# Performance work log

Hardware: AMD Instinct MI355X
Metric: run time of the kernel (lower is better)

## Reference

```python
import jax, jax.numpy as jnp
import numpy as np

N_NODES = 50000
N_EDGES = 800000
D = 256


def gcn_conv(x, edge_index, W, b, n_nodes):
    """PyG-style GCNConv: add self-loops, symmetric norm, linear, scatter-add."""
    # add self loops
    loops = jnp.arange(n_nodes, dtype=edge_index.dtype)
    src = jnp.concatenate([edge_index[0], loops])  # message sources
    dst = jnp.concatenate([edge_index[1], loops])  # aggregation targets
    # symmetric normalization: deg computed on targets (incl. self loops)
    deg = jax.ops.segment_sum(jnp.ones_like(dst, dtype=x.dtype), dst,
                              num_segments=n_nodes)
    dinv = jnp.where(deg > 0, jax.lax.rsqrt(deg), 0.0)
    norm = dinv[src] * dinv[dst]  # [E+N]
    h = x @ W  # [N, out]
    msg = h[src] * norm[:, None]  # gather + scale, [E+N, out]
    out = jax.ops.segment_sum(msg, dst, num_segments=n_nodes)  # scatter-add
    return out + b


def setup_inputs() -> dict:
    key = jax.random.key(0)
    k1, k2, k3, k4 = jax.random.split(key, 4)
    x = jax.random.normal(k1, (N_NODES, D), dtype=jnp.float32)
    edge_index = jax.random.randint(k2, (2, N_EDGES), 0, N_NODES, dtype=jnp.int64)
    s = 1.0 / np.sqrt(D)
    W1 = jax.random.normal(k3, (D, D), dtype=jnp.float32) * s
    W2 = jax.random.normal(k4, (D, D), dtype=jnp.float32) * s
    b1 = jnp.zeros((D,), dtype=jnp.float32)
    b2 = jnp.zeros((D,), dtype=jnp.float32)
    return {"x": x, "edge_index": edge_index, "W1": W1, "b1": b1,
            "W2": W2, "b2": b2}


def reference(x, edge_index, W1, b1, W2, b2):
    n = x.shape[0]
    out = gcn_conv(x, edge_index, W1, b1, n)
    out = jax.nn.relu(out)  # dropout is identity in eval mode (p=0.2 in train)
    out = out + gcn_conv(x, edge_index, W2, b2, n)
    return out
```

## Files before the change

### kernel.cpp

```cpp
#include <hip/hip_runtime.h>
#include <hip/hip_bf16.h>

#define DIM 256
#define CAP 64

typedef short bf16x8 __attribute__((ext_vector_type(8)));
typedef float f32x4  __attribute__((ext_vector_type(4)));

__device__ __forceinline__ unsigned short f2b(float f) {
    union { __hip_bfloat16 h; unsigned short u; } cv;
    cv.h = __float2bfloat16(f);
    return cv.u;
}
__device__ __forceinline__ float b2f(unsigned short u) {
    return __uint_as_float(((unsigned)u) << 16);
}

#define OFF_FILL   0
#define OFF_DINV   262144
#define OFF_WT1    524288
#define OFF_WT2    655360
#define OFF_BUCKET 786432
#define OFF_AGG    13631488
#define OFF_YB     39845888
#define NEED_BF    (OFF_YB + 25600000ull)

__global__ void k_fill(const int* __restrict__ src, const int* __restrict__ dst,
                       int* __restrict__ fill, int* __restrict__ bucket, int nE) {
    int e = blockIdx.x * blockDim.x + threadIdx.x;
    if (e < nE) {
        int d = dst[e];
        int pos = atomicAdd(&fill[d], 1);
        if (pos < CAP) bucket[d * CAP + pos] = src[e];
    }
}

__global__ void k_dinv(const int* __restrict__ fill, float* __restrict__ dinv, int n) {
    int i = blockIdx.x * blockDim.x + threadIdx.x;
    if (i < n) dinv[i] = rsqrtf((float)(1 + fill[i]));
}

__global__ void k_wt(const float* __restrict__ W1, const float* __restrict__ W2,
                     unsigned short* __restrict__ wt1, unsigned short* __restrict__ wt2) {
    int t = blockIdx.x * blockDim.x + threadIdx.x;
    if (t < DIM * DIM) {
        int k = t & 255, nn = t >> 8;
        wt1[t] = f2b(W1[k * DIM + nn]);
        wt2[t] = f2b(W2[k * DIM + nn]);
    }
}

__global__ void k_yb(const float4* __restrict__ x4, const float* __restrict__ dinv,
                     ushort4* __restrict__ yb, int n4) {
    int t = blockIdx.x * blockDim.x + threadIdx.x;
    if (t < n4) {
        float d = dinv[t >> 6];
        float4 v = x4[t];
        ushort4 r;
        r.x = f2b(d * v.x); r.y = f2b(d * v.y);
        r.z = f2b(d * v.z); r.w = f2b(d * v.w);
        yb[t] = r;
    }
}

__global__ void k_agg_bf(const ushort4* __restrict__ yb, const float* __restrict__ dinv,
                         const int* __restrict__ fill, const int* __restrict__ bucket,
                         ushort4* __restrict__ aggbf, int n) {
    int node = (blockIdx.x * blockDim.x + threadIdx.x) >> 6;
    int lane = threadIdx.x & 63;
    if (node >= n) return;

    ushort4 s = yb[(size_t)node * 64 + lane];
    float a0 = b2f(s.x), a1 = b2f(s.y), a2 = b2f(s.z), a3 = b2f(s.w);

    int c = fill[node];
    if (c > CAP) c = CAP;
    const int* bk = bucket + node * CAP;

    int k = 0;
    for (; k + 4 <= c; k += 4) {
        int4 j4 = *(const int4*)(bk + k);
        ushort4 r0 = yb[(size_t)j4.x * 64 + lane];
        ushort4 r1 = yb[(size_t)j4.y * 64 + lane];
        ushort4 r2 = yb[(size_t)j4.z * 64 + lane];
        ushort4 r3 = yb[(size_t)j4.w * 64 + lane];
        a0 += b2f(r0.x) + b2f(r1.x) + b2f(r2.x) + b2f(r3.x);
        a1 += b2f(r0.y) + b2f(r1.y) + b2f(r2.y) + b2f(r3.y);
        a2 += b2f(r0.z) + b2f(r1.z) + b2f(r2.z) + b2f(r3.z);
        a3 += b2f(r0.w) + b2f(r1.w) + b2f(r2.w) + b2f(r3.w);
    }
    for (; k < c; k++) {
        int j = bk[k];
        ushort4 r = yb[(size_t)j * 64 + lane];
        a0 += b2f(r.x); a1 += b2f(r.y); a2 += b2f(r.z); a3 += b2f(r.w);
    }

    float di = dinv[node];
    ushort4 r;
    r.x = f2b(a0 * di); r.y = f2b(a1 * di);
    r.z = f2b(a2 * di); r.w = f2b(a3 * di);
    unsigned long long rbits;
    __builtin_memcpy(&rbits, &r, 8);
    __builtin_nontemporal_store(rbits,
        (unsigned long long*)&aggbf[(size_t)node * 64 + lane]);
}

__global__ void k_agg_f32(const float4* __restrict__ x4, const float* __restrict__ dinv,
                          const int* __restrict__ fill, const int* __restrict__ bucket,
                          ushort4* __restrict__ aggbf, int n) {
    int node = (blockIdx.x * blockDim.x + threadIdx.x) >> 6;
    int lane = threadIdx.x & 63;
    if (node >= n) return;

    float di = dinv[node];
    float4 xi = x4[(size_t)node * 64 + lane];
    float a0 = di * xi.x, a1 = di * xi.y, a2 = di * xi.z, a3 = di * xi.w;

    int c = fill[node];
    if (c > CAP) c = CAP;
    const int* bk = bucket + node * CAP;
    for (int k = 0; k < c; k++) {
        int j = bk[k];
        float dj = dinv[j];
        float4 xj = x4[(size_t)j * 64 + lane];
        a0 += dj * xj.x; a1 += dj * xj.y; a2 += dj * xj.z; a3 += dj * xj.w;
    }
    ushort4 r;
    r.x = f2b(a0 * di); r.y = f2b(a1 * di);
    r.z = f2b(a2 * di); r.w = f2b(a3 * di);
    aggbf[(size_t)node * 64 + lane] = r;
}

__launch_bounds__(256, 2)
__global__ void k_gemm(const short* __restrict__ aggbf,
                       const short* __restrict__ wt1, const short* __restrict__ wt2,
                       const float* __restrict__ b1, const float* __restrict__ b2,
                       float* __restrict__ out, int n) {
    int mblk = blockIdx.x >> 1;
    int cb   = blockIdx.x & 1;
    int r0   = mblk * 64;
    int c0   = cb * 128;

    int wave = threadIdx.x >> 6;
    int lane = threadIdx.x & 63;
    int rowoff = (wave >> 1) * 32;
    int coloff = (wave & 1) * 64;
    int lrow = lane & 15;
    int quad = lane >> 4;

    int ar0 = r0 + rowoff + lrow;        if (ar0 >= n) ar0 = 0;
    int ar1 = r0 + rowoff + 16 + lrow;   if (ar1 >= n) ar1 = 0;
    const short* ap0 = aggbf + (size_t)ar0 * DIM + quad * 8;
    const short* ap1 = aggbf + (size_t)ar1 * DIM + quad * 8;

    const short* bp1[4];
    const short* bp2[4];
#pragma unroll
    for (int ct = 0; ct < 4; ct++) {
        int c = c0 + coloff + ct * 16 + lrow;
        bp1[ct] = wt1 + (size_t)c * DIM + quad * 8;
        bp2[ct] = wt2 + (size_t)c * DIM + quad * 8;
    }

    f32x4 acc1[2][4], acc2[2][4];
#pragma unroll
    for (int rt = 0; rt < 2; rt++)
#pragma unroll
        for (int ct = 0; ct < 4; ct++) {
            acc1[rt][ct] = (f32x4){0.f, 0.f, 0.f, 0.f};
            acc2[rt][ct] = (f32x4){0.f, 0.f, 0.f, 0.f};
        }

#pragma unroll
    for (int kk = 0; kk < DIM; kk += 32) {
        bf16x8 a0 = *(const bf16x8*)(ap0 + kk);
        bf16x8 a1 = *(const bf16x8*)(ap1 + kk);
#pragma unroll
        for (int ct = 0; ct < 4; ct++) {
            bf16x8 w1f = *(const bf16x8*)(bp1[ct] + kk);
            bf16x8 w2f = *(const bf16x8*)(bp2[ct] + kk);
            acc1[0][ct] = __builtin_amdgcn_mfma_f32_16x16x32_bf16(a0, w1f, acc1[0][ct], 0, 0, 0);
            acc1[1][ct] = __builtin_amdgcn_mfma_f32_16x16x32_bf16(a1, w1f, acc1[1][ct], 0, 0, 0);
            acc2[0][ct] = __builtin_amdgcn_mfma_f32_16x16x32_bf16(a0, w2f, acc2[0][ct], 0, 0, 0);
            acc2[1][ct] = __builtin_amdgcn_mfma_f32_16x16x32_bf16(a1, w2f, acc2[1][ct], 0, 0, 0);
        }
    }

#pragma unroll
    for (int ct = 0; ct < 4; ct++) {
        int col = c0 + coloff + ct * 16 + lrow;
        float bb1 = b1[col], bb2 = b2[col];
#pragma unroll
        for (int rt = 0; rt < 2; rt++) {
            int rbase = r0 + rowoff + rt * 16 + quad * 4;
#pragma unroll
            for (int i = 0; i < 4; i++) {
                int row = rbase + i;
                if (row < n) {
                    float v = fmaxf(acc1[rt][ct][i] + bb1, 0.f) + acc2[rt][ct][i] + bb2;
                    __builtin_nontemporal_store(v, &out[(size_t)row * DIM + col]);
                }
            }
        }
    }
}

extern "C" void kernel_launch(void* const* d_in, const int* in_sizes, int n_in,
                              void* d_out, int out_size, void* d_ws, size_t ws_size,
                              hipStream_t stream) {
    const float* x  = (const float*)d_in[0];
    const int*   ei = (const int*)d_in[1];
    const float* W1 = (const float*)d_in[2];
    const float* b1 = (const float*)d_in[3];
    const float* W2 = (const float*)d_in[4];
    const float* b2 = (const float*)d_in[5];
    float* out = (float*)d_out;

    int n = in_sizes[0] / DIM;
    int E = in_sizes[1] / 2;
    const int* src = ei;
    const int* dst = ei + E;

    char* ws = (char*)d_ws;
    int*            fill   = (int*)(ws + OFF_FILL);
    float*          dinv   = (float*)(ws + OFF_DINV);
    unsigned short* wt1    = (unsigned short*)(ws + OFF_WT1);
    unsigned short* wt2    = (unsigned short*)(ws + OFF_WT2);
    int*            bucket = (int*)(ws + OFF_BUCKET);
    ushort4*        aggbf  = (ushort4*)(ws + OFF_AGG);
    ushort4*        yb     = (ushort4*)(ws + OFF_YB);

    (void)hipMemsetAsync(fill, 0, n * sizeof(int), stream);

    k_fill<<<(E + 255) / 256, 256, 0, stream>>>(src, dst, fill, bucket, E);
    k_dinv<<<(n + 255) / 256, 256, 0, stream>>>(fill, dinv, n);
    k_wt  <<<(DIM * DIM + 255) / 256, 256, 0, stream>>>(W1, W2, wt1, wt2);

    int aggBlocks = (n * 64 + 255) / 256;
    bool use_bf = (ws_size >= NEED_BF);
    if (use_bf) {
        int n4 = n * DIM / 4;
        k_yb<<<(n4 + 255) / 256, 256, 0, stream>>>((const float4*)x, dinv, yb, n4);
        k_agg_bf<<<aggBlocks, 256, 0, stream>>>(yb, dinv, fill, bucket, aggbf, n);
    } else {
        k_agg_f32<<<aggBlocks, 256, 0, stream>>>((const float4*)x, dinv, fill, bucket, aggbf, n);
    }

    int mblocks = (n + 63) / 64;
    k_gemm<<<mblocks * 2, 256, 0, stream>>>((const short*)aggbf, (const short*)wt1,
                                            (const short*)wt2, b1, b2, out, n);
}
```

Baseline: 296.5 us.

## Stage weight slices in swizzled LDS and make GEMM persistent over row tiles

The GEMM kernel now loads a 64-column slice of both transposed weight matrices into LDS once per block, using an XOR swizzle to avoid bank conflicts. Each block then loops persistently over 128-row tiles with a grid of 128x4 blocks, and the A fragments for the next k-step are prefetched. This is meant to remove the repeated global/L2 weight fetches the old per-tile kernel issued, at the cost of 64KB of LDS per block and a fixed grid that may underfill the GPU or leave tiles unbalanced. The launch bounds also change to 4 blocks per CU.

```diff
diff --git a/kernel.cpp b/kernel.cpp
--- a/kernel.cpp
+++ b/kernel.cpp
@@ -3,6 +3,7 @@
 
 #define DIM 256
 #define CAP 64
+#define GEMM_G 128
 
 typedef short bf16x8 __attribute__((ext_vector_type(8)));
 typedef float f32x4  __attribute__((ext_vector_type(4)));
@@ -131,74 +132,94 @@
     aggbf[(size_t)node * 64 + lane] = r;
 }
 
-__launch_bounds__(256, 2)
+__launch_bounds__(256, 4)
 __global__ void k_gemm(const short* __restrict__ aggbf,
                        const short* __restrict__ wt1, const short* __restrict__ wt2,
                        const float* __restrict__ b1, const float* __restrict__ b2,
-                       float* __restrict__ out, int n) {
-    int mblk = blockIdx.x >> 1;
-    int cb   = blockIdx.x & 1;
-    int r0   = mblk * 64;
-    int c0   = cb * 128;
-
-    int wave = threadIdx.x >> 6;
-    int lane = threadIdx.x & 63;
-    int rowoff = (wave >> 1) * 32;
-    int coloff = (wave & 1) * 64;
+                       float* __restrict__ out, int n, int ntiles) {
+    __shared__ uint4 bs[4096];
+
+    int c0  = blockIdx.y * 64;
+    int tid = threadIdx.x;
+
+#pragma unroll
+    for (int i = 0; i < 16; i++) {
+        int l = tid + i * 256;
+        int m = l >> 11, rem = l & 2047, nn = rem >> 5, p = rem & 31;
+        const short* base = (m == 0) ? wt1 : wt2;
+        const uint4* sp = (const uint4*)(base + ((size_t)(c0 + nn)) * DIM) + p;
+        bs[(m << 11) + (nn << 5) + (p ^ (nn & 31))] = *sp;
+    }
+    __syncthreads();
+
+    int lane = tid & 63;
+    int wave = tid >> 6;
     int lrow = lane & 15;
     int quad = lane >> 4;
 
-    int ar0 = r0 + rowoff + lrow;        if (ar0 >= n) ar0 = 0;
-    int ar1 = r0 + rowoff + 16 + lrow;   if (ar1 >= n) ar1 = 0;
-    const short* ap0 = aggbf + (size_t)ar0 * DIM + quad * 8;
-    const short* ap1 = aggbf + (size_t)ar1 * DIM + quad * 8;
-
-    const short* bp1[4];
-    const short* bp2[4];
+    float bb1[4], bb2[4];
 #pragma unroll
     for (int ct = 0; ct < 4; ct++) {
-        int c = c0 + coloff + ct * 16 + lrow;
-        bp1[ct] = wt1 + (size_t)c * DIM + quad * 8;
-        bp2[ct] = wt2 + (size_t)c * DIM + quad * 8;
-    }
-
-    f32x4 acc1[2][4], acc2[2][4];
-#pragma unroll
-    for (int rt = 0; rt < 2; rt++)
-#pragma unroll
-        for (int ct = 0; ct < 4; ct++) {
-            acc1[rt][ct] = (f32x4){0.f, 0.f, 0.f, 0.f};
-            acc2[rt][ct] = (f32x4){0.f, 0.f, 0.f, 0.f};
+        bb1[ct] = b1[c0 + ct * 16 + lrow];
+        bb2[ct] = b2[c0 + ct * 16 + lrow];
+    }
+
+    for (int t = blockIdx.x; t < ntiles; t += gridDim.x) {
+        int rowbase = t * 128 + wave * 32;
+        int r0 = rowbase + lrow;       if (r0 >= n) r0 = 0;
+        int r1 = rowbase + 16 + lrow;  if (r1 >= n) r1 = 0;
+        const short* ap0 = aggbf + (size_t)r0 * DIM + quad * 8;
+        const short* ap1 = aggbf + (size_t)r1 * DIM + quad * 8;
+
+        f32x4 acc1[2][4], acc2[2][4];
+#pragma unroll
+        for (int sub = 0; sub < 2; sub++)
+#pragma unroll
+            for (int ct = 0; ct < 4; ct++) {
+                acc1[sub][ct] = (f32x4){0.f, 0.f, 0.f, 0.f};
+                acc2[sub][ct] = (f32x4){0.f, 0.f, 0.f, 0.f};
+            }
+
+        bf16x8 a0 = *(const bf16x8*)(ap0);
+        bf16x8 a1 = *(const bf16x8*)(ap1);
+#pragma unroll
+        for (int s = 0; s < 8; s++) {
+            bf16x8 na0 = a0, na1 = a1;
+            if (s < 7) {
+                na0 = *(const bf16x8*)(ap0 + (s + 1) * 32);
+                na1 = *(const bf16x8*)(ap1 + (s + 1) * 32);
+            }
+#pragma unroll
+            for (int ct = 0; ct < 4; ct++) {
+                int nn = ct * 16 + lrow;
+                int ch = (4 * s + quad) ^ (nn & 31);
+                uint4 u1 = bs[(nn << 5) + ch];
+                uint4 u2 = bs[2048 + (nn << 5) + ch];
+                bf16x8 w1f, w2f;
+                __builtin_memcpy(&w1f, &u1, 16);
+                __builtin_memcpy(&w2f, &u2, 16);
+                acc1[0][ct] = __builtin_amdgcn_mfma_f32_16x16x32_bf16(a0, w1f, acc1[0][ct], 0, 0, 0);
+                acc1[1][ct] = __builtin_amdgcn_mfma_f32_16x16x32_bf16(a1, w1f, acc1[1][ct], 0, 0, 0);
+                acc2[0][ct] = __builtin_amdgcn_mfma_f32_16x16x32_bf16(a0, w2f, acc2[0][ct], 0, 0, 0);
+                acc2[1][ct] = __builtin_amdgcn_mfma_f32_16x16x32_bf16(a1, w2f, acc2[1][ct], 0, 0, 0);
+            }
+            a0 = na0; a1 = na1;
         }
 
 #pragma unroll
-    for (int kk = 0; kk < DIM; kk += 32) {
-        bf16x8 a0 = *(const bf16x8*)(ap0 + kk);
-        bf16x8 a1 = *(const bf16x8*)(ap1 + kk);
-#pragma unroll
-        for (int ct = 0; ct < 4; ct++) {
-            bf16x8 w1f = *(const bf16x8*)(bp1[ct] + kk);
-            bf16x8 w2f = *(const bf16x8*)(bp2[ct] + kk);
-            acc1[0][ct] = __builtin_amdgcn_mfma_f32_16x16x32_bf16(a0, w1f, acc1[0][ct], 0, 0, 0);
-            acc1[1][ct] = __builtin_amdgcn_mfma_f32_16x16x32_bf16(a1, w1f, acc1[1][ct], 0, 0, 0);
-            acc2[0][ct] = __builtin_amdgcn_mfma_f32_16x16x32_bf16(a0, w2f, acc2[0][ct], 0, 0, 0);
-            acc2[1][ct] = __builtin_amdgcn_mfma_f32_16x16x32_bf16(a1, w2f, acc2[1][ct], 0, 0, 0);
-        }
-    }
-
-#pragma unroll
-    for (int ct = 0; ct < 4; ct++) {
-        int col = c0 + coloff + ct * 16 + lrow;
-        float bb1 = b1[col], bb2 = b2[col];
-#pragma unroll
-        for (int rt = 0; rt < 2; rt++) {
-            int rbase = r0 + rowoff + rt * 16 + quad * 4;
-#pragma unroll
-            for (int i = 0; i < 4; i++) {
-                int row = rbase + i;
-                if (row < n) {
-                    float v = fmaxf(acc1[rt][ct][i] + bb1, 0.f) + acc2[rt][ct][i] + bb2;
-                    __builtin_nontemporal_store(v, &out[(size_t)row * DIM + col]);
+        for (int sub = 0; sub < 2; sub++) {
+            int rb = rowbase + sub * 16 + quad * 4;
+#pragma unroll
+            for (int ct = 0; ct < 4; ct++) {
+                int col = c0 + ct * 16 + lrow;
+#pragma unroll
+                for (int i = 0; i < 4; i++) {
+                    int row = rb + i;
+                    if (row < n) {
+                        float v = fmaxf(acc1[sub][ct][i] + bb1[ct], 0.f)
+                                + acc2[sub][ct][i] + bb2[ct];
+                        __builtin_nontemporal_store(v, &out[(size_t)row * DIM + col]);
+                    }
                 }
             }
         }
@@ -246,7 +267,8 @@
         k_agg_f32<<<aggBlocks, 256, 0, stream>>>((const float4*)x, dinv, fill, bucket, aggbf, n);
     }
 
-    int mblocks = (n + 63) / 64;
-    k_gemm<<<mblocks * 2, 256, 0, stream>>>((const short*)aggbf, (const short*)wt1,
-                                            (const short*)wt2, b1, b2, out, n);
-}
+    int ntiles = (n + 127) / 128;
+    dim3 ggrid(GEMM_G, DIM / 64);
+    k_gemm<<<ggrid, 256, 0, stream>>>((const short*)aggbf, (const short*)wt1,
+                                      (const short*)wt2, b1, b2, out, n, ntiles);
+}
```

New measurement: 267.5 us. -9.8%, faster.
